# Kernel optimization log

Hardware: AMD Instinct MI355X
Metric: run time of the kernel (lower is better)

Reference implementation:

```python
import jax, jax.numpy as jnp
import numpy as np

GROUP_NUMS = 30
T_ITERS = 10
SIGMA = 0.01
SEED_THRESHOLD = 0.1


def _gumbel_topk(key, logits, k):
    # Sampling without replacement (torch.multinomial replacement=False) via Gumbel-top-k.
    u = jax.random.uniform(key, logits.shape, minval=1e-9, maxval=1.0)
    g = -jnp.log(-jnp.log(u))
    return jax.lax.top_k(logits + g, k)[1]


def _pairwise_dist(x):
    # x: [B,3,S] -> [B,S,S]
    return jnp.linalg.norm(x[:, :, :, None] - x[:, :, None, :], axis=1)


def _one_iterate(key, src_xyz, src_corr_xyz, weights, seed_nums, group_nums):
    B, _, N = src_xyz.shape
    S, G = seed_nums, group_nums
    k1, k2 = jax.random.split(key)
    # seed sampling without replacement, proportional to weights
    seed_idx = _gumbel_topk(k1, jnp.log(weights), S)                       # [B,S]
    seed_w = jnp.take_along_axis(weights, seed_idx, axis=-1)              # [B,S]
    idx3 = jnp.broadcast_to(seed_idx[:, None, :], (B, 3, S))
    seed_src = jnp.take_along_axis(src_xyz, idx3, axis=-1)                # [B,3,S]
    seed_corr = jnp.take_along_axis(src_corr_xyz, idx3, axis=-1)          # [B,3,S]
    # geometric consensus (no_grad in torch)
    cons = jnp.exp(-(_pairwise_dist(seed_src) - _pairwise_dist(seed_corr)) ** 2 / SIGMA)
    cons = jax.lax.stop_gradient(jnp.clip(cons, 0.1, None))               # [B,S,S]
    probs = cons / jnp.sum(cons, axis=-1, keepdims=True)
    nn_idx = _gumbel_topk(k2, jnp.log(probs), G)                          # [B,S,G]
    bidx = jnp.arange(B)[:, None, None]
    src_pts = seed_src.transpose(0, 2, 1)                                 # [B,S,3]
    corr_pts = seed_corr.transpose(0, 2, 1)
    src_nn = src_pts[bidx, nn_idx]                                        # [B,S,G,3]
    corr_nn = corr_pts[bidx, nn_idx]                                      # [B,S,G,3]
    w_nn = seed_w[bidx, nn_idx]                                           # [B,S,G]
    src2 = src_nn.transpose(0, 1, 3, 2).reshape(B * S, 3, G)
    corr2 = corr_nn.transpose(0, 1, 3, 2).reshape(B * S, 3, G)
    w2 = w_nn.reshape(B * S, G)
    w2 = w2 / jnp.sum(w2, axis=-1, keepdims=True)
    src_c = src2 - src2.mean(axis=2, keepdims=True)
    corr_c = corr2 - corr2.mean(axis=2, keepdims=True)
    H = jnp.matmul(src_c * w2[:, None, :], corr_c.transpose(0, 2, 1))     # [BS,3,3]
    U, _, Vh = jnp.linalg.svd(H)
    V = Vh.transpose(0, 2, 1)          # torch.svd returns V (not V^T)
    Ut = U.transpose(0, 2, 1)
    detv = jnp.linalg.det(jnp.matmul(V, Ut))                              # [BS]
    d = jnp.stack([jnp.ones_like(detv), jnp.ones_like(detv), detv], axis=-1)
    R = jnp.matmul(V * d[:, None, :], Ut)                                 # V @ diag(1,1,det) @ U^T
    t = jnp.matmul(-R, src2.mean(axis=2, keepdims=True)) + corr2.mean(axis=2, keepdims=True)  # [BS,3,1]
    R = R.reshape(B, S, 3, 3)
    t = t.reshape(B, S, 1, 3)
    pred = jnp.einsum('bsnm,bmk->bsnk', R, src_xyz) + t.transpose(0, 1, 3, 2)  # [B,S,3,N]
    L2 = jnp.linalg.norm(pred - src_corr_xyz[:, None, :, :], axis=-2)     # [B,S,N]
    fitness = jnp.mean((L2 < SEED_THRESHOLD).astype(jnp.float32), axis=-1)  # [B,S]
    best = jnp.argmax(fitness, axis=-1)                                   # [B]
    vv = jnp.mean(jnp.max(fitness, axis=-1))
    ba = jnp.arange(B)
    return vv, R[ba, best], t[ba, best]


def setup_inputs() -> dict:
    key = jax.random.key(0)
    k1, k2, k3 = jax.random.split(key, 3)
    B, N = 8, 2048
    src_xyz = jax.random.normal(k1, (B, 3, N), dtype=jnp.float32)
    tgt_xyz = jax.random.normal(k2, (B, 3, N), dtype=jnp.float32)
    weights = jax.random.normal(k3, (B, N), dtype=jnp.float32)
    return {"src_xyz": src_xyz, "tgt_xyz": tgt_xyz, "weights": weights}


def reference(src_xyz, tgt_xyz, weights):
    key = jax.random.key(42)
    w = jnp.where(jnp.isnan(weights), jnp.float32(1e-7), weights)
    w = jnp.where(jnp.isinf(w), jnp.float32(1.0), w)
    seed_nums = w.shape[-1] // 2
    w = jax.nn.softmax(w, axis=-1)
    B = src_xyz.shape[0]
    dist = jnp.float32(1e8)
    Rs = jnp.zeros((B, 3, 3), jnp.float32)
    ts = jnp.zeros((B, 1, 3), jnp.float32)
    for it in range(T_ITERS):
        vv, fR, ft = _one_iterate(jax.random.fold_in(key, it), src_xyz, tgt_xyz, w, seed_nums, GROUP_NUMS)
        better = vv < dist
        Rs = jnp.where(better, fR, Rs)
        ts = jnp.where(better, ft, ts)
        dist = jnp.where(better, vv, dist)
    return Rs, ts[:, 0, :]
```

## Files before the change

### kernel.cpp

```cpp
#include <hip/hip_runtime.h>
#include <stdint.h>
#include <math.h>

#pragma clang fp contract(off)

#define NB    8
#define NPTS  2048
#define NS    1024
#define NG    30
#define NITER 10

typedef unsigned long long ull;

__host__ __device__ __forceinline__ uint32_t rotl32(uint32_t x, int r){
  return (x << r) | (x >> (32 - r));
}
__host__ __device__ __forceinline__ void tf2x32(uint32_t k0, uint32_t k1,
                                                uint32_t x0, uint32_t x1,
                                                uint32_t& o0, uint32_t& o1){
  uint32_t k2 = k0 ^ k1 ^ 0x1BD11BDAu;
  x0 += k0; x1 += k1;
#define TFR(r) { x0 += x1; x1 = rotl32(x1, (r)); x1 ^= x0; }
  TFR(13) TFR(15) TFR(26) TFR(6)
  x0 += k1; x1 += k2 + 1u;
  TFR(17) TFR(29) TFR(16) TFR(24)
  x0 += k2; x1 += k0 + 2u;
  TFR(13) TFR(15) TFR(26) TFR(6)
  x0 += k0; x1 += k1 + 3u;
  TFR(17) TFR(29) TFR(16) TFR(24)
  x0 += k1; x1 += k2 + 4u;
  TFR(13) TFR(15) TFR(26) TFR(6)
  x0 += k2; x1 += k0 + 5u;
#undef TFR
  o0 = x0; o1 = x1;
}

__device__ __forceinline__ uint32_t rand_bits(uint32_t k0, uint32_t k1, uint32_t e){
  uint32_t o0, o1; tf2x32(k0, k1, 0u, e, o0, o1);
  return o0 ^ o1;
}

__device__ __forceinline__ void derive_key(int it, uint32_t which,
                                           uint32_t& a, uint32_t& b){
  uint32_t fa, fb;
  tf2x32(0u, 42u, 0u, (uint32_t)it, fa, fb);
  tf2x32(fa, fb, 0u, which, a, b);
}

__device__ __forceinline__ float gumbel_from(uint32_t bits){
  float f = __uint_as_float((bits >> 9) | 0x3f800000u) - 1.0f;
  float u = fmaxf(1e-9f, f + 1e-9f);
  return -logf(-logf(u));
}

__device__ __forceinline__ ull packkey(float v, uint32_t idx){
  uint32_t u = __float_as_uint(v);
  u = (u & 0x80000000u) ? ~u : (u | 0x80000000u);
  return ((ull)u << 32) | (ull)(0xFFFFFFFFu - idx);
}
__device__ __forceinline__ uint32_t unpackidx(ull k){
  return 0xFFFFFFFFu - (uint32_t)(k & 0xFFFFFFFFull);
}

__device__ __forceinline__ void bitonic_desc(ull* a, int M, int t, int T){
  for (int k = 2; k <= M; k <<= 1){
    for (int j = k >> 1; j > 0; j >>= 1){
      for (int i = t; i < M; i += T){
        int ixj = i ^ j;
        if (ixj > i){
          ull ai = a[i], aj = a[ixj];
          bool desc = ((i & k) == 0);
          if (desc ? (ai < aj) : (ai > aj)){ a[i] = aj; a[ixj] = ai; }
        }
      }
      __syncthreads();
    }
  }
}

__device__ __forceinline__ ull shfl_xor_u64(ull x, int mask){
  return (ull)__shfl_xor((long long)x, mask, 64);
}

__device__ __forceinline__ ull sort32_desc(ull key, int l){
  int i = l & 31;
#pragma unroll
  for (int k = 2; k <= 16; k <<= 1){
#pragma unroll
    for (int j = k >> 1; j > 0; j >>= 1){
      ull other = shfl_xor_u64(key, j);
      bool up = ((l & j) == 0);
      bool take_max = (((i & k) == 0) == up);
      bool omax = other > key;
      key = (take_max == omax) ? other : key;
    }
  }
#pragma unroll
  for (int j = 16; j > 0; j >>= 1){
    ull other = shfl_xor_u64(key, j);
    bool up = ((l & j) == 0);
    bool omax = other > key;
    key = (up == omax) ? other : key;
  }
  return key;
}

__device__ __forceinline__ ull merge64_desc(ull key, int l){
#pragma unroll
  for (int j = 32; j > 0; j >>= 1){
    ull other = shfl_xor_u64(key, j);
    bool up = ((l & j) == 0);
    bool omax = other > key;
    key = (up == omax) ? other : key;
  }
  return key;
}

__device__ __forceinline__ ull mergehalves_desc(ull key, int l){
  ull rev = shfl_xor_u64(key, 31);
  if (l >= 32) key = rev;
  return merge64_desc(key, l);
}

__global__ __launch_bounds__(256) void ghv_softmax(const float* __restrict__ win,
                                                   float* __restrict__ w,
                                                   float* __restrict__ logw){
  int b = blockIdx.x, t = threadIdx.x;
  __shared__ float sh[NPTS];
  __shared__ float red[4];
  __shared__ float bcast;
  for (int n = t; n < NPTS; n += 256){
    float x = win[b*NPTS + n];
    if (isnan(x)) x = 1e-7f;
    if (isinf(x)) x = 1.0f;
    sh[n] = x;
  }
  __syncthreads();
  float m = -INFINITY;
  for (int n = t; n < NPTS; n += 256) m = fmaxf(m, sh[n]);
  for (int off = 32; off >= 1; off >>= 1) m = fmaxf(m, __shfl_down(m, off));
  if ((t & 63) == 0) red[t >> 6] = m;
  __syncthreads();
  if (t == 0) bcast = fmaxf(fmaxf(red[0], red[1]), fmaxf(red[2], red[3]));
  __syncthreads();
  float mx = bcast;
  float ss = 0.0f;
  for (int n = t; n < NPTS; n += 256){ float e = expf(sh[n] - mx); sh[n] = e; ss += e; }
  for (int off = 32; off >= 1; off >>= 1) ss += __shfl_down(ss, off);
  if ((t & 63) == 0) red[t >> 6] = ss;
  __syncthreads();
  if (t == 0) bcast = red[0] + red[1] + red[2] + red[3];
  __syncthreads();
  float tot = bcast;
  for (int n = t; n < NPTS; n += 256){
    float wv = sh[n] / tot;
    w[b*NPTS + n] = wv;
    logw[b*NPTS + n] = logf(wv);
  }
}

__global__ __launch_bounds__(1024) void ghv_seed(const float* __restrict__ src,
                                                 const float* __restrict__ tgt,
                                                 const float* __restrict__ w,
                                                 const float* __restrict__ logw,
                                                 float* __restrict__ seeds,
                                                 int it0, int seq){
  __shared__ ull keys[NPTS];
  __shared__ uint32_t kk[2];
  int b = blockIdx.x, t = threadIdx.x;
  int it = it0 + blockIdx.z;
  int slot = seq ? 0 : it;
  if (t == 0){ derive_key(it, 0u, kk[0], kk[1]); }
  __syncthreads();
  uint32_t k0 = kk[0], k1 = kk[1];
  for (int n = t; n < NPTS; n += 1024){
    uint32_t bits = rand_bits(k0, k1, (uint32_t)(b*NPTS + n));
    float v = logw[b*NPTS + n] + gumbel_from(bits);
    keys[n] = packkey(v, (uint32_t)n);
  }
  __syncthreads();
  bitonic_desc(keys, NPTS, t, 1024);
  int s = t;
  uint32_t idx = unpackidx(keys[s]);
  const float* sb = src + b*3*NPTS;
  const float* tb = tgt + b*3*NPTS;
  float* sp = seeds + (size_t)slot*(NB*NS*8) + (size_t)((b << 10) + s) * 8;
  sp[0] = sb[idx]; sp[1] = sb[NPTS + idx]; sp[2] = sb[2*NPTS + idx];
  sp[3] = tb[idx]; sp[4] = tb[NPTS + idx]; sp[5] = tb[2*NPTS + idx];
  sp[6] = w[b*NPTS + idx]; sp[7] = 0.0f;
}

__global__ __launch_bounds__(512) void ghv_nn(const float* __restrict__ seeds,
                                              unsigned short* __restrict__ nnb,
                                              int it0, int seq){
  __shared__ ull UN[1024];
  __shared__ ull sbuf[256];
  __shared__ ull sbuf2[128];
  __shared__ unsigned short candi[512];
  __shared__ float red[8];
  __shared__ float srow[8];
  __shared__ float rowsum_sh;
  __shared__ uint32_t cmax32[32];
  __shared__ uint32_t fT_sh;
  __shared__ int wcnt[8];
  __shared__ uint32_t kk[2];

  float* cons_sh = (float*)UN;
  ull* kbuf = UN + 512;

  int s = blockIdx.x, b = blockIdx.y, t = threadIdx.x;
  int it = it0 + blockIdx.z;
  int slot = seq ? 0 : it;
  const float* sdat = seeds + (size_t)slot*(NB*NS*8);
  size_t outoff = ((size_t)slot*(NB*NS) + (size_t)((b << 10) + s))*32;
  int wv = t >> 6, l = t & 63;

  if (t < 8) srow[t] = sdat[(size_t)((b << 10) + s)*8 + t];
  if (t == 0){ derive_key(it, 1u, kk[0], kk[1]); }
  __syncthreads();
  uint32_t k0 = kk[0], k1 = kk[1];
  ull ltm = (l == 0) ? 0ull : ((1ull << l) - 1ull);
  uint32_t eb = (uint32_t)((b << 20) + (s << 10));

  float consr[2]; bool clipped[2]; uint32_t bitsr[2];
  float part = 0.0f;
#pragma unroll
  for (int q = 0; q < 2; ++q){
    int j = t + q*512;
    const float4* jp = (const float4*)(sdat + (size_t)((b << 10) + j)*8);
    float4 p0 = jp[0], p1 = jp[1];
    float dxs = srow[0]-p0.x, dys = srow[1]-p0.y, dzs = srow[2]-p0.z;
    float ds  = sqrtf(dxs*dxs + dys*dys + dzs*dzs);
    float dxc = srow[3]-p0.w, dyc = srow[4]-p1.x, dzc = srow[5]-p1.y;
    float dc  = sqrtf(dxc*dxc + dyc*dyc + dzc*dzc);
    float diff = ds - dc;
    float arg = (-(diff*diff)) / 0.01f;
    clipped[q] = (arg < -2.3026f);
    float cons = fmaxf(expf(arg), 0.1f);
    consr[q] = cons;
    cons_sh[j] = cons;
    bitsr[q] = rand_bits(k0, k1, eb + (uint32_t)j);
    part += cons;
  }

  for (int off = 32; off >= 1; off >>= 1) part += __shfl_down(part, off);
  if ((t & 63) == 0) red[t >> 6] = part;
  __syncthreads();
  if (t == 0){ float tot = 0.0f; for (int i = 0; i < 8; ++i) tot += red[i]; rowsum_sh = tot; }
  __syncthreads();
  float rowsum = rowsum_sh;

#pragma unroll
  for (int q = 0; q < 2; ++q){
    uint32_t m = clipped[q] ? (bitsr[q] >> 9) : 0u;
#pragma unroll
    for (int d = 1; d <= 16; d <<= 1){
      uint32_t o = (uint32_t)__shfl_xor((int)m, d);
      m = (o > m) ? o : m;
    }
    if ((l & 31) == 0) cmax32[(q << 4) + (t >> 5)] = m;
  }
  __syncthreads();
  if (t < 32){
    uint32_t m = cmax32[t];
#pragma unroll
    for (int d = 1; d <= 16; d <<= 1){
      uint32_t o = (uint32_t)__shfl_xor((int)m, d);
      m = (o < m) ? o : m;
    }
    if (t == 0) fT_sh = m;
  }
  __syncthreads();
  uint32_t fT = fT_sh;

  bool cand0 = (!clipped[0]) || ((bitsr[0] >> 9) >= fT);
  bool cand1 = (!clipped[1]) || ((bitsr[1] >> 9) >= fT);
  ull m0 = __ballot(cand0), m1 = __ballot(cand1);
  int c0 = __popcll(m0), c1 = __popcll(m1);
  if (l == 0) wcnt[wv] = c0 + c1;
  __syncthreads();
  int base = 0, ncand = 0;
#pragma unroll
  for (int i = 0; i < 8; ++i){
    int c = wcnt[i];
    if (i < wv) base += c;
    ncand += c;
  }
  if (cand0){
    int pos = base + __popcll(m0 & ltm);
    if (pos < 512) candi[pos] = (unsigned short)t;
  }
  if (cand1){
    int pos = base + c0 + __popcll(m1 & ltm);
    if (pos < 512) candi[pos] = (unsigned short)(t + 512);
  }
  __syncthreads();

  if (ncand <= 512){
    ull kkey = 0ull;
    if (t < ncand){
      int j = candi[t];
      uint32_t bits = rand_bits(k0, k1, eb + (uint32_t)j);
      float v = logf(cons_sh[j] / rowsum) + gumbel_from(bits);
      kkey = packkey(v, (uint32_t)j);
    }
    if (wv * 64 < ncand){
      kkey = sort32_desc(kkey, l);
      kkey = mergehalves_desc(kkey, l);
    }
    if (l < 32) sbuf[(wv << 5) + l] = kkey;
    __syncthreads();
    if (wv < 4){
      ull k2 = 0ull;
      if (wv * 128 < ncand){
        k2 = (l < 32) ? sbuf[(wv << 6) + l] : sbuf[(wv << 6) + 95 - l];
        k2 = merge64_desc(k2, l);
      }
      if (l < 32) sbuf2[(wv << 5) + l] = k2;
    }
    __syncthreads();
    if (wv < 2){
      ull k2 = (l < 32) ? sbuf2[(wv << 6) + l] : sbuf2[(wv << 6) + 95 - l];
      k2 = merge64_desc(k2, l);
      if (l < 32) sbuf[(wv << 5) + l] = k2;
    }
    __syncthreads();
    if (wv == 0){
      ull k2 = (l < 32) ? sbuf[l] : sbuf[95 - l];
      k2 = merge64_desc(k2, l);
      if (l < 32) nnb[outoff + l] = (l < NG) ? (unsigned short)unpackidx(k2) : 0;
    }
  } else {
    float v0 = logf(consr[0] / rowsum) + gumbel_from(bitsr[0]);
    float v1 = logf(consr[1] / rowsum) + gumbel_from(bitsr[1]);
    ull key0 = packkey(v0, (uint32_t)t);
    ull key1 = packkey(v1, (uint32_t)(t + 512));
    __syncthreads();
    UN[t] = key0; UN[t + 512] = key1;
    __syncthreads();
    bitonic_desc(UN, NS, t, 512);
    if (t < 32) nnb[outoff + t] = (t < NG) ? (unsigned short)unpackidx(UN[t]) : 0;
  }
}

__global__ __launch_bounds__(64) void ghv_kabsch(const float* __restrict__ seeds,
                                                 const unsigned short* __restrict__ nnb,
                                                 float* __restrict__ Rt,
                                                 int it0, int seq){
  int id = blockIdx.x*64 + threadIdx.x;
  int it = it0 + blockIdx.z;
  int slot = seq ? 0 : it;
  int b = id >> 10;
  const float* sdat = seeds + (size_t)slot*(NB*NS*8);
  const unsigned short* nnp = nnb + ((size_t)slot*(NB*NS) + (size_t)id)*32;

  float sxs=0, sys=0, szs=0, cxs=0, cys=0, czs=0, wsum=0;
  for (int g = 0; g < NG; ++g){
    int j = nnp[g];
    const float4* jp = (const float4*)(sdat + (size_t)((b << 10) + j)*8);
    float4 p0 = jp[0], p1 = jp[1];
    sxs += p0.x; sys += p0.y; szs += p0.z;
    cxs += p0.w; cys += p1.x; czs += p1.y;
    wsum += p1.z;
  }
  float msx = sxs/30.0f, msy = sys/30.0f, msz = szs/30.0f;
  float mcx = cxs/30.0f, mcy = cys/30.0f, mcz = czs/30.0f;

  float Hf[9] = {0,0,0,0,0,0,0,0,0};
  for (int g = 0; g < NG; ++g){
    int j = nnp[g];
    const float4* jp = (const float4*)(sdat + (size_t)((b << 10) + j)*8);
    float4 p0 = jp[0], p1 = jp[1];
    float wg = p1.z / wsum;
    float a0 = p0.x - msx, a1 = p0.y - msy, a2 = p0.z - msz;
    float b0 = p0.w - mcx, b1 = p1.x - mcy, b2 = p1.y - mcz;
    float a0w = a0*wg, a1w = a1*wg, a2w = a2*wg;
    Hf[0] += a0w*b0; Hf[1] += a0w*b1; Hf[2] += a0w*b2;
    Hf[3] += a1w*b0; Hf[4] += a1w*b1; Hf[5] += a1w*b2;
    Hf[6] += a2w*b0; Hf[7] += a2w*b1; Hf[8] += a2w*b2;
  }

  double H[9]; for (int i = 0; i < 9; ++i) H[i] = (double)Hf[i];
  double A[3][3];
  A[0][0] = H[0]*H[0] + H[3]*H[3] + H[6]*H[6];
  A[0][1] = H[0]*H[1] + H[3]*H[4] + H[6]*H[7];
  A[0][2] = H[0]*H[2] + H[3]*H[5] + H[6]*H[8];
  A[1][1] = H[1]*H[1] + H[4]*H[4] + H[7]*H[7];
  A[1][2] = H[1]*H[2] + H[4]*H[5] + H[7]*H[8];
  A[2][2] = H[2]*H[2] + H[5]*H[5] + H[8]*H[8];
  A[1][0] = A[0][1]; A[2][0] = A[0][2]; A[2][1] = A[1][2];
  double V[3][3] = {{1,0,0},{0,1,0},{0,0,1}};
  for (int sw = 0; sw < 8; ++sw){
    for (int p = 0; p < 2; ++p){
      for (int q = p+1; q < 3; ++q){
        double apq = A[p][q];
        if (fabs(apq) > 1e-300){
          double th = (A[q][q] - A[p][p]) / (2.0*apq);
          double tt = copysign(1.0, th) / (fabs(th) + sqrt(1.0 + th*th));
          double c  = 1.0 / sqrt(1.0 + tt*tt), sn = tt*c;
          int r = 3 - p - q;
          double app = A[p][p], aqq = A[q][q];
          double arp = A[r][p], arq = A[r][q];
          A[p][p] = app - tt*apq;
          A[q][q] = aqq + tt*apq;
          A[p][q] = 0.0; A[q][p] = 0.0;
          A[r][p] = c*arp - sn*arq; A[p][r] = A[r][p];
          A[r][q] = sn*arp + c*arq; A[q][r] = A[r][q];
          for (int kk = 0; kk < 3; ++kk){
            double vp = V[kk][p], vq = V[kk][q];
            V[kk][p] = c*vp - sn*vq;
            V[kk][q] = sn*vp + c*vq;
          }
        }
      }
    }
  }
  int o0 = 0, o1 = 1, o2 = 2;
  double l0 = A[0][0], l1 = A[1][1], l2 = A[2][2];
  double tmp; int ti;
  if (l0 < l1){ tmp=l0; l0=l1; l1=tmp; ti=o0; o0=o1; o1=ti; }
  if (l0 < l2){ tmp=l0; l0=l2; l2=tmp; ti=o0; o0=o2; o2=ti; }
  if (l1 < l2){ tmp=l1; l1=l2; l2=tmp; ti=o1; o1=o2; o2=ti; }
  double v0[3] = {V[0][o0], V[1][o0], V[2][o0]};
  double v1[3] = {V[0][o1], V[1][o1], V[2][o1]};
  double v2[3] = {V[0][o2], V[1][o2], V[2][o2]};

  double u0[3], u1[3], u2[3];
  for (int i = 0; i < 3; ++i) u0[i] = H[i*3+0]*v0[0] + H[i*3+1]*v0[1] + H[i*3+2]*v0[2];
  double n0 = sqrt(u0[0]*u0[0] + u0[1]*u0[1] + u0[2]*u0[2]);
  if (n0 > 1e-150){ u0[0]/=n0; u0[1]/=n0; u0[2]/=n0; }
  else { u0[0]=1; u0[1]=0; u0[2]=0; }
  for (int i = 0; i < 3; ++i) u1[i] = H[i*3+0]*v1[0] + H[i*3+1]*v1[1] + H[i*3+2]*v1[2];
  double d01 = u0[0]*u1[0] + u0[1]*u1[1] + u0[2]*u1[2];
  for (int i = 0; i < 3; ++i) u1[i] -= d01*u0[i];
  double n1 = sqrt(u1[0]*u1[0] + u1[1]*u1[1] + u1[2]*u1[2]);
  if (n1 > 1e-150){ u1[0]/=n1; u1[1]/=n1; u1[2]/=n1; }
  else {
    double ax = fabs(u0[0]), ay = fabs(u0[1]), az = fabs(u0[2]);
    double e[3] = {0,0,0};
    if (ax <= ay && ax <= az) e[0] = 1; else if (ay <= az) e[1] = 1; else e[2] = 1;
    double de = u0[0]*e[0] + u0[1]*e[1] + u0[2]*e[2];
    for (int i = 0; i < 3; ++i) u1[i] = e[i] - de*u0[i];
    double nn1 = sqrt(u1[0]*u1[0] + u1[1]*u1[1] + u1[2]*u1[2]);
    for (int i = 0; i < 3; ++i) u1[i] /= nn1;
  }
  u2[0] = u0[1]*u1[2] - u0[2]*u1[1];
  u2[1] = u0[2]*u1[0] - u0[0]*u1[2];
  u2[2] = u0[0]*u1[1] - u0[1]*u1[0];
  double detV = v0[0]*(v1[1]*v2[2] - v1[2]*v2[1])
              - v0[1]*(v1[0]*v2[2] - v1[2]*v2[0])
              + v0[2]*(v1[0]*v2[1] - v1[1]*v2[0]);
  float Rf[9];
  for (int i = 0; i < 3; ++i)
    for (int j = 0; j < 3; ++j)
      Rf[i*3+j] = (float)(v0[i]*u0[j] + v1[i]*u1[j] + detV*(v2[i]*u2[j]));
  float tx = -(Rf[0]*msx + Rf[1]*msy + Rf[2]*msz) + mcx;
  float ty = -(Rf[3]*msx + Rf[4]*msy + Rf[5]*msz) + mcy;
  float tz = -(Rf[6]*msx + Rf[7]*msy + Rf[8]*msz) + mcz;
  float* o = Rt + ((size_t)slot*(NB*NS) + (size_t)id)*12;
  for (int i = 0; i < 9; ++i) o[i] = Rf[i];
  o[9] = tx; o[10] = ty; o[11] = tz;
}

__global__ __launch_bounds__(256) void ghv_fitness(const float* __restrict__ src,
                                                   const float* __restrict__ tgt,
                                                   const float* __restrict__ Rt,
                                                   int* __restrict__ fit){
  __shared__ float Pf[12288];
  int b = blockIdx.y, t = threadIdx.x;
  int slot = blockIdx.z;
  int s0 = blockIdx.x * 16;
  const float4* g4s = (const float4*)(src + (size_t)b*3*NPTS);
  const float4* g4t = (const float4*)(tgt + (size_t)b*3*NPTS);
  float4* l4 = (float4*)Pf;
  for (int i = t; i < 1536; i += 256){
    l4[i] = g4s[i];
    l4[1536 + i] = g4t[i];
  }
  __syncthreads();
  int wv = t >> 6, l = t & 63;
  for (int k = 0; k < 4; ++k){
    int s = s0 + wv*4 + k;
    size_t id = (size_t)slot*(NB*NS) + (size_t)((b << 10) + s);
    const float* rt = Rt + id*12;
    float R0 = rt[0], R1 = rt[1], R2 = rt[2];
    float R3 = rt[3], R4 = rt[4], R5 = rt[5];
    float R6 = rt[6], R7 = rt[7], R8 = rt[8];
    float t0 = rt[9], t1 = rt[10], t2 = rt[11];
    int cnt = 0;
    for (int n = l; n < NPTS; n += 64){
      float x = Pf[n], y = Pf[2048 + n], z = Pf[4096 + n];
      float px = R0*x + R1*y + R2*z + t0;
      float py = R3*x + R4*y + R5*z + t1;
      float pz = R6*x + R7*y + R8*z + t2;
      float dx = px - Pf[6144 + n], dy = py - Pf[8192 + n], dz = pz - Pf[10240 + n];
      float l2 = sqrtf(dx*dx + dy*dy + dz*dz);
      cnt += (l2 < 0.1f) ? 1 : 0;
    }
    for (int off = 32; off >= 1; off >>= 1) cnt += __shfl_down(cnt, off);
    if (l == 0) fit[id] = cnt;
  }
}

__global__ __launch_bounds__(512) void ghv_select_b(const float* __restrict__ Rt,
                                                    const int* __restrict__ fit,
                                                    float* __restrict__ out){
  __shared__ int mc[NITER*NB], mi[NITER*NB];
  __shared__ int best_sh;
  int t = threadIdx.x;
  int w = t >> 6, l = t & 63;
  for (int task = w; task < NITER*NB; task += 8){
    int it = task >> 3, b = task & 7;
    int bc = -1, bi = 0;
    const int* fp = fit + (size_t)it*(NB*NS) + (b << 10);
    for (int s = l; s < NS; s += 64){
      int c = fp[s];
      if (c > bc){ bc = c; bi = s; }
    }
    for (int off = 32; off >= 1; off >>= 1){
      int oc = __shfl_down(bc, off);
      int oi = __shfl_down(bi, off);
      if (oc > bc || (oc == bc && oi < bi)){ bc = oc; bi = oi; }
    }
    if (l == 0){ mc[task] = bc; mi[task] = bi; }
  }
  __syncthreads();
  if (t == 0){
    float dist = 1e8f;
    int best = 0;
    for (int it = 0; it < NITER; ++it){
      int sum = 0;
      for (int b = 0; b < NB; ++b) sum += mc[(it << 3) + b];
      float vv = (float)sum / 16384.0f;
      if (vv < dist){ dist = vv; best = it; }
    }
    best_sh = best;
  }
  __syncthreads();
  int bit = best_sh;
  for (int i = t; i < 96; i += 512){
    float v;
    if (i < 72){
      int bb = i / 9, k = i % 9;
      v = Rt[((size_t)bit*(NB*NS) + (size_t)((bb << 10) + mi[(bit << 3) + bb]))*12 + k];
    } else {
      int ii = i - 72; int bb = ii / 3, k = ii % 3;
      v = Rt[((size_t)bit*(NB*NS) + (size_t)((bb << 10) + mi[(bit << 3) + bb]))*12 + 9 + k];
    }
    out[i] = v;
  }
}

__global__ __launch_bounds__(512) void ghv_select_s(const float* __restrict__ Rt,
                                                    const int* __restrict__ fit,
                                                    float* __restrict__ dist_ws,
                                                    float* __restrict__ out,
                                                    int first){
  __shared__ int mc[8], mi[8];
  __shared__ int flag;
  int t = threadIdx.x;
  int b = t >> 6, lane = t & 63;
  int bc = -1, bi = 0;
  for (int s = lane; s < NS; s += 64){
    int c = fit[(b << 10) + s];
    if (c > bc){ bc = c; bi = s; }
  }
  for (int off = 32; off >= 1; off >>= 1){
    int oc = __shfl_down(bc, off);
    int oi = __shfl_down(bi, off);
    if (oc > bc || (oc == bc && oi < bi)){ bc = oc; bi = oi; }
  }
  if (lane == 0){ mc[b] = bc; mi[b] = bi; }
  __syncthreads();
  if (t == 0){
    int sum = 0; for (int i = 0; i < 8; ++i) sum += mc[i];
    float vv = (float)sum / 16384.0f;
    float dist = first ? 1e8f : dist_ws[0];
    int better = (vv < dist) ? 1 : 0;
    if (better) dist_ws[0] = vv;
    flag = better;
  }
  __syncthreads();
  if (flag){
    for (int i = t; i < 96; i += 512){
      float v;
      if (i < 72){
        int bb = i / 9, k = i % 9;
        v = Rt[(size_t)((bb << 10) + mi[bb])*12 + k];
      } else {
        int ii = i - 72; int bb = ii / 3, k = ii % 3;
        v = Rt[(size_t)((bb << 10) + mi[bb])*12 + 9 + k];
      }
      out[i] = v;
    }
  }
}

extern "C" void kernel_launch(void* const* d_in, const int* in_sizes, int n_in,
                              void* d_out, int out_size, void* d_ws, size_t ws_size,
                              hipStream_t stream){
  const float* src = (const float*)d_in[0];
  const float* tgt = (const float*)d_in[1];
  const float* win = (const float*)d_in[2];
  float* out = (float*)d_out;
  char* ws = (char*)d_ws;

  const size_t SEEDS_SZ = (size_t)NB*NS*8*4;
  const size_t RT_SZ    = (size_t)NB*NS*12*4;
  const size_t NN_SZ    = (size_t)NB*NS*32*2;
  const size_t FIT_SZ   = (size_t)NB*NS*4;
  const size_t W_SZ     = (size_t)NB*NPTS*4;

  size_t off_w    = 0;
  size_t off_logw = off_w + W_SZ;
  size_t off_seed = off_logw + W_SZ;
  size_t off_Rt   = off_seed + NITER*SEEDS_SZ;
  size_t off_nn   = off_Rt + NITER*RT_SZ;
  size_t off_fit  = off_nn + NITER*NN_SZ;
  size_t need_b   = off_fit + NITER*FIT_SZ;

  if (ws_size >= need_b){
    float* w     = (float*)(ws + off_w);
    float* logw  = (float*)(ws + off_logw);
    float* seeds = (float*)(ws + off_seed);
    float* Rt    = (float*)(ws + off_Rt);
    unsigned short* nnb = (unsigned short*)(ws + off_nn);
    int*   fit   = (int*)(ws + off_fit);

    ghv_softmax<<<NB, 256, 0, stream>>>(win, w, logw);
    ghv_seed   <<<dim3(NB, 1, NITER), 1024, 0, stream>>>(src, tgt, w, logw, seeds, 0, 0);
    ghv_nn     <<<dim3(NS, NB, NITER), 512, 0, stream>>>(seeds, nnb, 0, 0);
    ghv_kabsch <<<dim3(NB*NS/64, 1, NITER), 64, 0, stream>>>(seeds, nnb, Rt, 0, 0);
    ghv_fitness<<<dim3(NS/16, NB, NITER), 256, 0, stream>>>(src, tgt, Rt, fit);
    ghv_select_b<<<1, 512, 0, stream>>>(Rt, fit, out);
  } else {
    size_t o_w = 0, o_lw = W_SZ, o_sd = 2*W_SZ, o_rt = o_sd + SEEDS_SZ,
           o_nn2 = o_rt + RT_SZ, o_ft = o_nn2 + NN_SZ, o_ds = o_ft + FIT_SZ;
    float* w     = (float*)(ws + o_w);
    float* logw  = (float*)(ws + o_lw);
    float* seeds = (float*)(ws + o_sd);
    float* Rt    = (float*)(ws + o_rt);
    unsigned short* nnb = (unsigned short*)(ws + o_nn2);
    int*   fit   = (int*)(ws + o_ft);
    float* dist  = (float*)(ws + o_ds);

    ghv_softmax<<<NB, 256, 0, stream>>>(win, w, logw);
    for (int it = 0; it < NITER; ++it){
      ghv_seed   <<<dim3(NB, 1, 1), 1024, 0, stream>>>(src, tgt, w, logw, seeds, it, 1);
      ghv_nn     <<<dim3(NS, NB, 1), 512, 0, stream>>>(seeds, nnb, it, 1);
      ghv_kabsch <<<dim3(NB*NS/64, 1, 1), 64, 0, stream>>>(seeds, nnb, Rt, it, 1);
      ghv_fitness<<<dim3(NS/16, NB, 1), 256, 0, stream>>>(src, tgt, Rt, fit);
      ghv_select_s<<<1, 512, 0, stream>>>(Rt, fit, dist, out, (it == 0) ? 1 : 0);
    }
  }
}
```

Before: 951.5 us.

## Compute exp only for unclipped consensus entries and verify candidate top-k

The neighbour kernel now calls exp only for unclipped entries and treats clipped entries as the constant 0.1. It splits candidates into unclipped and threshold-passing clipped groups and checks whether the 30th key ties the minimum clipped key, falling back to a full bitonic sort if so. The Jacobi sweep count in the Kabsch SVD drops from 8 to 6, and the fitness kernel handles 32 seeds per block instead of 16. Fewer sweeps risk less accurate rotations, and the candidate logic adds extra barriers and shared memory.

```diff
diff --git a/kernel.cpp b/kernel.cpp
--- a/kernel.cpp
+++ b/kernel.cpp
@@ -193,20 +193,23 @@
 __global__ __launch_bounds__(512) void ghv_nn(const float* __restrict__ seeds,
                                               unsigned short* __restrict__ nnb,
                                               int it0, int seq){
-  __shared__ ull UN[1024];
+  __shared__ ull BIG[1024];
   __shared__ ull sbuf[256];
   __shared__ ull sbuf2[128];
+  __shared__ float argc[512];
   __shared__ unsigned short candi[512];
   __shared__ float red[8];
   __shared__ float srow[8];
-  __shared__ float rowsum_sh;
+  __shared__ float rowsum_sh, base_sh;
   __shared__ uint32_t cmax32[32];
   __shared__ uint32_t fT_sh;
-  __shared__ int wcnt[8];
+  __shared__ int wcA[8], wcB[8];
+  __shared__ uint32_t vminw[8];
+  __shared__ int flag_sh;
   __shared__ uint32_t kk[2];
 
-  float* cons_sh = (float*)UN;
-  ull* kbuf = UN + 512;
+  float* cons_sh = (float*)BIG;
+  uint32_t* ubits_sh = (uint32_t*)(BIG + 512);
 
   int s = blockIdx.x, b = blockIdx.y, t = threadIdx.x;
   int it = it0 + blockIdx.z;
@@ -222,8 +225,7 @@
   ull ltm = (l == 0) ? 0ull : ((1ull << l) - 1ull);
   uint32_t eb = (uint32_t)((b << 20) + (s << 10));
 
-  float consr[2]; bool clipped[2]; uint32_t bitsr[2];
-  float part = 0.0f;
+  float argr[2]; bool clipd[2]; uint32_t bitsr[2];
 #pragma unroll
   for (int q = 0; q < 2; ++q){
     int j = t + q*512;
@@ -235,24 +237,17 @@
     float dc  = sqrtf(dxc*dxc + dyc*dyc + dzc*dzc);
     float diff = ds - dc;
     float arg = (-(diff*diff)) / 0.01f;
-    clipped[q] = (arg < -2.3026f);
-    float cons = fmaxf(expf(arg), 0.1f);
-    consr[q] = cons;
-    cons_sh[j] = cons;
-    bitsr[q] = rand_bits(k0, k1, eb + (uint32_t)j);
-    part += cons;
-  }
-
-  for (int off = 32; off >= 1; off >>= 1) part += __shfl_down(part, off);
-  if ((t & 63) == 0) red[t >> 6] = part;
-  __syncthreads();
-  if (t == 0){ float tot = 0.0f; for (int i = 0; i < 8; ++i) tot += red[i]; rowsum_sh = tot; }
-  __syncthreads();
-  float rowsum = rowsum_sh;
+    argr[q] = arg;
+    clipd[q] = (arg < -2.3026f);
+    uint32_t bits = rand_bits(k0, k1, eb + (uint32_t)j);
+    bitsr[q] = bits;
+    ubits_sh[j] = bits;
+    cons_sh[j] = 0.1f;
+  }
 
 #pragma unroll
   for (int q = 0; q < 2; ++q){
-    uint32_t m = clipped[q] ? (bitsr[q] >> 9) : 0u;
+    uint32_t m = clipd[q] ? (bitsr[q] >> 9) : 0u;
 #pragma unroll
     for (int d = 1; d <= 16; d <<= 1){
       uint32_t o = (uint32_t)__shfl_xor((int)m, d);
@@ -273,73 +268,137 @@
   __syncthreads();
   uint32_t fT = fT_sh;
 
-  bool cand0 = (!clipped[0]) || ((bitsr[0] >> 9) >= fT);
-  bool cand1 = (!clipped[1]) || ((bitsr[1] >> 9) >= fT);
-  ull m0 = __ballot(cand0), m1 = __ballot(cand1);
-  int c0 = __popcll(m0), c1 = __popcll(m1);
-  if (l == 0) wcnt[wv] = c0 + c1;
-  __syncthreads();
-  int base = 0, ncand = 0;
+  bool cA0 = !clipd[0], cA1 = !clipd[1];
+  bool cB0 = clipd[0] && ((bitsr[0] >> 9) >= fT);
+  bool cB1 = clipd[1] && ((bitsr[1] >> 9) >= fT);
+  ull a0 = __ballot(cA0), a1 = __ballot(cA1);
+  ull b0 = __ballot(cB0), b1 = __ballot(cB1);
+  if (l == 0){ wcA[wv] = __popcll(a0) + __popcll(a1); wcB[wv] = __popcll(b0) + __popcll(b1); }
+  __syncthreads();
+  int ncu = 0, nS = 0, baseA = 0, baseB = 0;
 #pragma unroll
   for (int i = 0; i < 8; ++i){
-    int c = wcnt[i];
-    if (i < wv) base += c;
-    ncand += c;
-  }
-  if (cand0){
-    int pos = base + __popcll(m0 & ltm);
-    if (pos < 512) candi[pos] = (unsigned short)t;
-  }
-  if (cand1){
-    int pos = base + c0 + __popcll(m1 & ltm);
-    if (pos < 512) candi[pos] = (unsigned short)(t + 512);
-  }
-  __syncthreads();
-
-  if (ncand <= 512){
-    ull kkey = 0ull;
-    if (t < ncand){
-      int j = candi[t];
-      uint32_t bits = rand_bits(k0, k1, eb + (uint32_t)j);
-      float v = logf(cons_sh[j] / rowsum) + gumbel_from(bits);
-      kkey = packkey(v, (uint32_t)j);
-    }
-    if (wv * 64 < ncand){
-      kkey = sort32_desc(kkey, l);
-      kkey = mergehalves_desc(kkey, l);
-    }
-    if (l < 32) sbuf[(wv << 5) + l] = kkey;
+    int ca = wcA[i], cb = wcB[i];
+    if (i < wv){ baseA += ca; baseB += cb; }
+    ncu += ca; nS += cb;
+  }
+  int ncand = ncu + nS;
+
+  if (ncu > 512 || ncand > 512){
+    float c0 = fmaxf(expf(argr[0]), 0.1f);
+    float c1 = fmaxf(expf(argr[1]), 0.1f);
+    float part = c0 + c1;
+    for (int off = 32; off >= 1; off >>= 1) part += __shfl_down(part, off);
+    if ((t & 63) == 0) red[t >> 6] = part;
     __syncthreads();
-    if (wv < 4){
-      ull k2 = 0ull;
-      if (wv * 128 < ncand){
-        k2 = (l < 32) ? sbuf[(wv << 6) + l] : sbuf[(wv << 6) + 95 - l];
-        k2 = merge64_desc(k2, l);
-      }
-      if (l < 32) sbuf2[(wv << 5) + l] = k2;
-    }
+    if (t == 0){ float tot = 0.0f; for (int i = 0; i < 8; ++i) tot += red[i]; rowsum_sh = tot; }
     __syncthreads();
-    if (wv < 2){
-      ull k2 = (l < 32) ? sbuf2[(wv << 6) + l] : sbuf2[(wv << 6) + 95 - l];
-      k2 = merge64_desc(k2, l);
-      if (l < 32) sbuf[(wv << 5) + l] = k2;
-    }
-    __syncthreads();
-    if (wv == 0){
-      ull k2 = (l < 32) ? sbuf[l] : sbuf[95 - l];
-      k2 = merge64_desc(k2, l);
-      if (l < 32) nnb[outoff + l] = (l < NG) ? (unsigned short)unpackidx(k2) : 0;
-    }
-  } else {
-    float v0 = logf(consr[0] / rowsum) + gumbel_from(bitsr[0]);
-    float v1 = logf(consr[1] / rowsum) + gumbel_from(bitsr[1]);
+    float rowsum = rowsum_sh;
+    float v0 = logf(c0 / rowsum) + gumbel_from(bitsr[0]);
+    float v1 = logf(c1 / rowsum) + gumbel_from(bitsr[1]);
     ull key0 = packkey(v0, (uint32_t)t);
     ull key1 = packkey(v1, (uint32_t)(t + 512));
     __syncthreads();
-    UN[t] = key0; UN[t + 512] = key1;
+    BIG[t] = key0; BIG[t + 512] = key1;
     __syncthreads();
-    bitonic_desc(UN, NS, t, 512);
-    if (t < 32) nnb[outoff + t] = (t < NG) ? (unsigned short)unpackidx(UN[t]) : 0;
+    bitonic_desc(BIG, NS, t, 512);
+    if (t < 32) nnb[outoff + t] = (t < NG) ? (unsigned short)unpackidx(BIG[t]) : 0;
+    return;
+  }
+
+  if (cA0){ int p = baseA + __popcll(a0 & ltm); candi[p] = (unsigned short)t; argc[p] = argr[0]; }
+  if (cA1){ int p = baseA + __popcll(a0) + __popcll(a1 & ltm); candi[p] = (unsigned short)(t + 512); argc[p] = argr[1]; }
+  if (cB0){ int p = ncu + baseB + __popcll(b0 & ltm); candi[p] = (unsigned short)t; }
+  if (cB1){ int p = ncu + baseB + __popcll(b0) + __popcll(b1 & ltm); candi[p] = (unsigned short)(t + 512); }
+  __syncthreads();
+
+  if (t < ncu){
+    float c = fmaxf(expf(argc[t]), 0.1f);
+    cons_sh[candi[t]] = c;
+  }
+  __syncthreads();
+
+  float part = cons_sh[t] + cons_sh[t + 512];
+  for (int off = 32; off >= 1; off >>= 1) part += __shfl_down(part, off);
+  if ((t & 63) == 0) red[t >> 6] = part;
+  __syncthreads();
+  if (t == 0){
+    float tot = 0.0f; for (int i = 0; i < 8; ++i) tot += red[i];
+    rowsum_sh = tot;
+    base_sh = logf(0.1f / tot);
+  }
+  __syncthreads();
+  float rowsum = rowsum_sh, base = base_sh;
+
+  ull kkey = 0ull;
+  uint32_t mymin = 0xFFFFFFFFu;
+  if (t < ncand){
+    int j = candi[t];
+    uint32_t bits = ubits_sh[j];
+    float g = gumbel_from(bits);
+    float v;
+    if (t < ncu) v = logf(cons_sh[j] / rowsum) + g;
+    else         v = base + g;
+    kkey = packkey(v, (uint32_t)j);
+    if (t >= ncu) mymin = (uint32_t)(kkey >> 32);
+  }
+#pragma unroll
+  for (int d = 1; d <= 32; d <<= 1){
+    uint32_t o = (uint32_t)__shfl_xor((int)mymin, d);
+    mymin = (o < mymin) ? o : mymin;
+  }
+  if (l == 0) vminw[wv] = mymin;
+
+  if (wv * 64 < ncand){
+    kkey = sort32_desc(kkey, l);
+    kkey = mergehalves_desc(kkey, l);
+  }
+  if (l < 32) sbuf[(wv << 5) + l] = kkey;
+  __syncthreads();
+  if (wv < 4){
+    ull k2 = 0ull;
+    if (wv * 128 < ncand){
+      k2 = (l < 32) ? sbuf[(wv << 6) + l] : sbuf[(wv << 6) + 95 - l];
+      k2 = merge64_desc(k2, l);
+    }
+    if (l < 32) sbuf2[(wv << 5) + l] = k2;
+  }
+  __syncthreads();
+  if (wv < 2){
+    ull k2 = (l < 32) ? sbuf2[(wv << 6) + l] : sbuf2[(wv << 6) + 95 - l];
+    k2 = merge64_desc(k2, l);
+    if (l < 32) sbuf[(wv << 5) + l] = k2;
+  }
+  __syncthreads();
+  if (wv == 0){
+    ull k2 = (l < 32) ? sbuf[l] : sbuf[95 - l];
+    k2 = merge64_desc(k2, l);
+    if (l < 32) sbuf2[l] = k2;
+    ull k29 = (ull)__shfl((long long)k2, 29, 64);
+    if (l == 0){
+      uint32_t val29 = (uint32_t)(k29 >> 32);
+      uint32_t vm = 0xFFFFFFFFu;
+      for (int i = 0; i < 8; ++i) vm = (vminw[i] < vm) ? vminw[i] : vm;
+      flag_sh = (val29 == vm) ? 1 : 0;
+    }
+  }
+  __syncthreads();
+
+  if (!flag_sh){
+    if (t < 32) nnb[outoff + t] = (t < NG) ? (unsigned short)unpackidx(sbuf2[t]) : 0;
+  } else {
+    float c0f = cons_sh[t], c1f = cons_sh[t + 512];
+    uint32_t bb0 = ubits_sh[t], bb1 = ubits_sh[t + 512];
+    float g0 = gumbel_from(bb0), g1 = gumbel_from(bb1);
+    float v0 = (c0f == 0.1f) ? (base + g0) : (logf(c0f / rowsum) + g0);
+    float v1 = (c1f == 0.1f) ? (base + g1) : (logf(c1f / rowsum) + g1);
+    ull key0 = packkey(v0, (uint32_t)t);
+    ull key1 = packkey(v1, (uint32_t)(t + 512));
+    __syncthreads();
+    BIG[t] = key0; BIG[t + 512] = key1;
+    __syncthreads();
+    bitonic_desc(BIG, NS, t, 512);
+    if (t < 32) nnb[outoff + t] = (t < NG) ? (unsigned short)unpackidx(BIG[t]) : 0;
   }
 }
 
@@ -390,7 +449,7 @@
   A[2][2] = H[2]*H[2] + H[5]*H[5] + H[8]*H[8];
   A[1][0] = A[0][1]; A[2][0] = A[0][2]; A[2][1] = A[1][2];
   double V[3][3] = {{1,0,0},{0,1,0},{0,0,1}};
-  for (int sw = 0; sw < 8; ++sw){
+  for (int sw = 0; sw < 6; ++sw){
     for (int p = 0; p < 2; ++p){
       for (int q = p+1; q < 3; ++q){
         double apq = A[p][q];
@@ -469,7 +528,7 @@
   __shared__ float Pf[12288];
   int b = blockIdx.y, t = threadIdx.x;
   int slot = blockIdx.z;
-  int s0 = blockIdx.x * 16;
+  int s0 = blockIdx.x * 32;
   const float4* g4s = (const float4*)(src + (size_t)b*3*NPTS);
   const float4* g4t = (const float4*)(tgt + (size_t)b*3*NPTS);
   float4* l4 = (float4*)Pf;
@@ -479,8 +538,8 @@
   }
   __syncthreads();
   int wv = t >> 6, l = t & 63;
-  for (int k = 0; k < 4; ++k){
-    int s = s0 + wv*4 + k;
+  for (int k = 0; k < 8; ++k){
+    int s = s0 + wv*8 + k;
     size_t id = (size_t)slot*(NB*NS) + (size_t)((b << 10) + s);
     const float* rt = Rt + id*12;
     float R0 = rt[0], R1 = rt[1], R2 = rt[2];
@@ -631,7 +690,7 @@
     ghv_seed   <<<dim3(NB, 1, NITER), 1024, 0, stream>>>(src, tgt, w, logw, seeds, 0, 0);
     ghv_nn     <<<dim3(NS, NB, NITER), 512, 0, stream>>>(seeds, nnb, 0, 0);
     ghv_kabsch <<<dim3(NB*NS/64, 1, NITER), 64, 0, stream>>>(seeds, nnb, Rt, 0, 0);
-    ghv_fitness<<<dim3(NS/16, NB, NITER), 256, 0, stream>>>(src, tgt, Rt, fit);
+    ghv_fitness<<<dim3(NS/32, NB, NITER), 256, 0, stream>>>(src, tgt, Rt, fit);
     ghv_select_b<<<1, 512, 0, stream>>>(Rt, fit, out);
   } else {
     size_t o_w = 0, o_lw = W_SZ, o_sd = 2*W_SZ, o_rt = o_sd + SEEDS_SZ,
@@ -649,7 +708,7 @@
       ghv_seed   <<<dim3(NB, 1, 1), 1024, 0, stream>>>(src, tgt, w, logw, seeds, it, 1);
       ghv_nn     <<<dim3(NS, NB, 1), 512, 0, stream>>>(seeds, nnb, it, 1);
       ghv_kabsch <<<dim3(NB*NS/64, 1, 1), 64, 0, stream>>>(seeds, nnb, Rt, it, 1);
-      ghv_fitness<<<dim3(NS/16, NB, 1), 256, 0, stream>>>(src, tgt, Rt, fit);
+      ghv_fitness<<<dim3(NS/32, NB, 1), 256, 0, stream>>>(src, tgt, Rt, fit);
       ghv_select_s<<<1, 512, 0, stream>>>(Rt, fit, dist, out, (it == 0) ? 1 : 0);
     }
   }
```

Measured after the change: 964.3 us. About the same (+1.3%).
